# Kernel optimization log

Hardware: AMD Instinct MI355X
Metric: run time of the kernel (lower is better)

## Reference

```python
import jax, jax.numpy as jnp
import numpy as np

HEADS = 16

def setup_inputs() -> dict:
    key = jax.random.key(0)
    k1, k2, k3 = jax.random.split(key, 3)
    B, S, D = 4, 2048, 1024
    x = jax.random.normal(k1, (B, S, D), dtype=jnp.float32)
    w_qkv = jax.random.normal(k2, (D, 3 * D), dtype=jnp.float32) * (D ** -0.5)
    w_out = jax.random.normal(k3, (D, D), dtype=jnp.float32) * (D ** -0.5)
    return {"x": x, "w_qkv": w_qkv, "w_out": w_out}

def reference(x, w_qkv, w_out):
    B, S, D = x.shape
    H = HEADS
    hd = D // H
    qkv = jnp.einsum("bsd,de->bse", x, w_qkv)  # [B,S,3D]
    q, k, v = jnp.split(qkv, 3, axis=-1)
    # [B,S,D] -> [B,H,S,hd]
    q = q.reshape(B, S, H, hd).transpose(0, 2, 1, 3)
    k = k.reshape(B, S, H, hd).transpose(0, 2, 1, 3)
    v = v.reshape(B, S, H, hd).transpose(0, 2, 1, 3)
    scores = jnp.einsum("bhqd,bhkd->bhqk", q, k) / jnp.sqrt(jnp.float32(hd))
    attn = jax.nn.softmax(scores, axis=-1)
    out = jnp.einsum("bhqk,bhkd->bhqd", attn, v)  # [B,H,S,hd]
    out = out.transpose(0, 2, 1, 3).reshape(B, S, D)
    return jnp.einsum("bsd,de->bse", out, w_out)
```

## Files before the change

kernel.cpp:

```cpp
#include <hip/hip_runtime.h>

typedef __bf16 bf16;
typedef __bf16 bfx8 __attribute__((ext_vector_type(8)));
typedef __bf16 bfx4 __attribute__((ext_vector_type(4)));
typedef float f32x4 __attribute__((ext_vector_type(4)));

#define MFMA_BF16 __builtin_amdgcn_mfma_f32_16x16x32_bf16

static constexpr int Bq = 4, Sq = 2048, Dq = 1024, Hq = 16, HDq = 64;
static constexpr int Mq = Bq * Sq;
static constexpr int D3 = 3 * Dq;
static constexpr float L2E = 1.4426950408889634f;
static constexpr float QSC = 0.125f * L2E;

typedef const __attribute__((address_space(1))) void* gas1;
typedef __attribute__((address_space(3))) void* las3;

__device__ __forceinline__ void gload_lds16(const bf16* g, bf16* l) {
    __builtin_amdgcn_global_load_lds((gas1)g, (las3)l, 16, 0, 0);
}

__device__ __forceinline__ float fast_exp2(float x) {
    return __builtin_amdgcn_exp2f(x);
}

__global__ __launch_bounds__(256) void cast_f32_bf16(const float* __restrict__ in,
                                                     bf16* __restrict__ out, int n) {
    int i = (blockIdx.x * 256 + threadIdx.x) * 4;
    if (i + 3 < n) {
        float4 v = *(const float4*)(in + i);
        bfx4 r;
        r[0] = (bf16)v.x; r[1] = (bf16)v.y; r[2] = (bf16)v.z; r[3] = (bf16)v.w;
        *(bfx4*)(out + i) = r;
    }
}

__global__ __launch_bounds__(256) void transpose_cast(const float* __restrict__ in,
                                                      bf16* __restrict__ out, int R, int C) {
    __shared__ float tile[32][33];
    int tx = threadIdx.x, ty = threadIdx.y;
    int c0 = blockIdx.x * 32, r0 = blockIdx.y * 32;
    for (int j = 0; j < 32; j += 8)
        tile[ty + j][tx] = in[(size_t)(r0 + ty + j) * C + c0 + tx];
    __syncthreads();
    for (int j = 0; j < 32; j += 8)
        out[(size_t)(c0 + ty + j) * R + r0 + tx] = (bf16)tile[tx][ty + j];
}

__global__ __launch_bounds__(256) void vtrans(const bf16* __restrict__ qkv,
                                              bf16* __restrict__ Vt) {
    __shared__ bf16 tile[32][33];
    int tx = threadIdx.x, ty = threadIdx.y;
    int c0 = blockIdx.x * 32;
    int s0 = blockIdx.y * 32;
    int b = blockIdx.z;
    for (int j = 0; j < 32; j += 8)
        tile[ty + j][tx] = qkv[(size_t)(b * Sq + s0 + ty + j) * D3 + 2 * Dq + c0 + tx];
    __syncthreads();
    for (int j = 0; j < 32; j += 8)
        Vt[((size_t)b * Dq + c0 + ty + j) * Sq + s0 + tx] = tile[tx][ty + j];
}

template <bool OUT_F32, bool QSCALE>
__global__ __launch_bounds__(256) void gemm_bt(const bf16* __restrict__ A,
                                               const bf16* __restrict__ Bt,
                                               void* __restrict__ Cout,
                                               int M, int N, int K) {
    __shared__ bf16 As[128 * 64];
    __shared__ bf16 Bs[128 * 64];
    int m0 = blockIdx.y * 128;
    int n0 = blockIdx.x * 128;
    int tid = threadIdx.x;
    int lane = tid & 63, wave = tid >> 6;
    int quad = lane >> 4, l16 = lane & 15;
    int wr = wave >> 1, wc = wave & 1;
    int sw = l16 & 7;

    f32x4 acc[4][4] = {};

    for (int k0 = 0; k0 < K; k0 += 64) {
        __syncthreads();
        #pragma unroll
        for (int i = 0; i < 4; i++) {
            int c = i * 256 + tid;
            int row = c >> 3;
            int ch = (c & 7) ^ (row & 7);
            gload_lds16(A + (size_t)(m0 + row) * K + k0 + ch * 8, As + c * 8);
            gload_lds16(Bt + (size_t)(n0 + row) * K + k0 + ch * 8, Bs + c * 8);
        }
        __syncthreads();
        #pragma unroll
        for (int s = 0; s < 2; s++) {
            bfx8 af[4], bfr[4];
            #pragma unroll
            for (int i = 0; i < 4; i++)
                af[i] = *(const bfx8*)(As + (wr * 64 + i * 16 + l16) * 64 +
                                       ((s * 4 + quad) ^ sw) * 8);
            #pragma unroll
            for (int j = 0; j < 4; j++)
                bfr[j] = *(const bfx8*)(Bs + (wc * 64 + j * 16 + l16) * 64 +
                                        ((s * 4 + quad) ^ sw) * 8);
            #pragma unroll
            for (int i = 0; i < 4; i++)
                #pragma unroll
                for (int j = 0; j < 4; j++)
                    acc[i][j] = MFMA_BF16(af[i], bfr[j], acc[i][j], 0, 0, 0);
        }
    }

    #pragma unroll
    for (int i = 0; i < 4; i++)
        #pragma unroll
        for (int j = 0; j < 4; j++) {
            int col = n0 + wc * 64 + j * 16 + l16;
            float scale = (QSCALE && col < Dq) ? QSC : 1.0f;
            #pragma unroll
            for (int r = 0; r < 4; r++) {
                int row = m0 + wr * 64 + i * 16 + quad * 4 + r;
                if (OUT_F32)
                    ((float*)Cout)[(size_t)row * N + col] = acc[i][j][r];
                else
                    ((bf16*)Cout)[(size_t)row * N + col] = (bf16)(acc[i][j][r] * scale);
            }
        }
}

__global__ __launch_bounds__(256, 2) void attn_kernel(const bf16* __restrict__ qkv,
                                                      const bf16* __restrict__ Vt,
                                                      bf16* __restrict__ out) {
    __shared__ bf16 Ks[2][64 * 64];
    __shared__ bf16 Vs[2][64 * 64];
    __shared__ bf16 Ps[4][64 * 64];

    int bid = blockIdx.x;
    int qc = (bid >> 3) & 7;
    int head = (bid & 7) + ((bid >> 6) << 3);
    int h = head & 15, b = head >> 4;
    int tid = threadIdx.x;
    int lane = tid & 63, wave = tid >> 6;
    int quad = lane >> 4, l16 = lane & 15;
    int sw = l16 & 7;

    size_t base = (size_t)b * Sq * D3;
    const bf16* Kbase = qkv + base + Dq + h * HDq;
    const bf16* Vbase = Vt + ((size_t)b * Dq + h * HDq) * Sq;
    int q0 = qc * 256 + wave * 64;

    bfx8 qf[4][2];
    #pragma unroll
    for (int qt = 0; qt < 4; qt++)
        #pragma unroll
        for (int s = 0; s < 2; s++)
            qf[qt][s] = *(const bfx8*)(qkv + base + (size_t)(q0 + qt * 16 + l16) * D3 +
                                       h * HDq + s * 32 + quad * 8);

    bfx8 ones;
    #pragma unroll
    for (int j = 0; j < 8; j++) ones[j] = (bf16)1.0f;

    f32x4 oacc[4][4] = {};
    f32x4 lacc[4] = {};

    int c0 = tid, c1 = tid + 256;
    int r0 = c0 >> 3, ch0 = (c0 & 7) ^ (r0 & 7);
    int r1 = c1 >> 3, ch1 = (c1 & 7) ^ (r1 & 7);

    gload_lds16(Kbase + (size_t)r0 * D3 + ch0 * 8, Ks[0] + c0 * 8);
    gload_lds16(Vbase + (size_t)r0 * Sq + ch0 * 8, Vs[0] + c0 * 8);
    gload_lds16(Kbase + (size_t)r1 * D3 + ch1 * 8, Ks[0] + c1 * 8);
    gload_lds16(Vbase + (size_t)r1 * Sq + ch1 * 8, Vs[0] + c1 * 8);

    for (int i = 0; i < 32; i++) {
        int cur = i & 1;
        __syncthreads();
        if (i + 1 < 32) {
            int k0 = (i + 1) * 64;
            bf16* kd = Ks[cur ^ 1];
            bf16* vd = Vs[cur ^ 1];
            gload_lds16(Kbase + (size_t)(k0 + r0) * D3 + ch0 * 8, kd + c0 * 8);
            gload_lds16(Vbase + (size_t)r0 * Sq + k0 + ch0 * 8, vd + c0 * 8);
            gload_lds16(Kbase + (size_t)(k0 + r1) * D3 + ch1 * 8, kd + c1 * 8);
            gload_lds16(Vbase + (size_t)r1 * Sq + k0 + ch1 * 8, vd + c1 * 8);
        }
        const bf16* K_ = Ks[cur];
        const bf16* V_ = Vs[cur];

        bfx8 kf[4][2];
        #pragma unroll
        for (int t = 0; t < 4; t++) {
            kf[t][0] = *(const bfx8*)(K_ + (t * 16 + l16) * 64 + (quad ^ sw) * 8);
            kf[t][1] = *(const bfx8*)(K_ + (t * 16 + l16) * 64 + ((4 + quad) ^ sw) * 8);
        }

        #pragma unroll
        for (int qt = 0; qt < 4; qt++) {
            f32x4 s[4] = {};
            #pragma unroll
            for (int t = 0; t < 4; t++) {
                s[t] = MFMA_BF16(kf[t][0], qf[qt][0], s[t], 0, 0, 0);
                s[t] = MFMA_BF16(kf[t][1], qf[qt][1], s[t], 0, 0, 0);
            }
            #pragma unroll
            for (int t = 0; t < 4; t++) {
                bfx4 pk;
                #pragma unroll
                for (int r = 0; r < 4; r++)
                    pk[r] = (bf16)fast_exp2(s[t][r]);
                int slot = (2 * t + (quad >> 1)) ^ sw;
                *(bfx4*)(&Ps[wave][(qt * 16 + l16) * 64 + slot * 8 + (quad & 1) * 4]) = pk;
            }
        }

        bfx8 pf[4][2];
        #pragma unroll
        for (int qt = 0; qt < 4; qt++) {
            pf[qt][0] = *(const bfx8*)(&Ps[wave][(qt * 16 + l16) * 64 + (quad ^ sw) * 8]);
            pf[qt][1] = *(const bfx8*)(&Ps[wave][(qt * 16 + l16) * 64 + ((4 + quad) ^ sw) * 8]);
            lacc[qt] = MFMA_BF16(pf[qt][0], ones, lacc[qt], 0, 0, 0);
            lacc[qt] = MFMA_BF16(pf[qt][1], ones, lacc[qt], 0, 0, 0);
        }

        #pragma unroll
        for (int nt = 0; nt < 4; nt++) {
            bfx8 vf0 = *(const bfx8*)(V_ + (nt * 16 + l16) * 64 + (quad ^ sw) * 8);
            bfx8 vf1 = *(const bfx8*)(V_ + (nt * 16 + l16) * 64 + ((4 + quad) ^ sw) * 8);
            #pragma unroll
            for (int qt = 0; qt < 4; qt++) {
                oacc[qt][nt] = MFMA_BF16(pf[qt][0], vf0, oacc[qt][nt], 0, 0, 0);
                oacc[qt][nt] = MFMA_BF16(pf[qt][1], vf1, oacc[qt][nt], 0, 0, 0);
            }
        }
    }

    #pragma unroll
    for (int qt = 0; qt < 4; qt++)
        #pragma unroll
        for (int r = 0; r < 4; r++) {
            int row = q0 + qt * 16 + quad * 4 + r;
            float inv = 1.0f / lacc[qt][r];
            #pragma unroll
            for (int nt = 0; nt < 4; nt++)
                out[((size_t)b * Sq + row) * Dq + h * HDq + nt * 16 + l16] =
                    (bf16)(oacc[qt][nt][r] * inv);
        }
}

extern "C" void kernel_launch(void* const* d_in, const int* in_sizes, int n_in,
                              void* d_out, int out_size, void* d_ws, size_t ws_size,
                              hipStream_t stream) {
    const float* x     = (const float*)d_in[0];
    const float* w_qkv = (const float*)d_in[1];
    const float* w_out = (const float*)d_in[2];
    float* out = (float*)d_out;

    char* ws = (char*)d_ws;
    bf16* x_bf   = (bf16*)ws;
    bf16* wqkvT  = (bf16*)(ws + 16777216);
    bf16* woutT  = (bf16*)(ws + 16777216 + 6291456);
    bf16* qkv    = (bf16*)(ws + 16777216 + 6291456 + 2097152);
    bf16* attn   = (bf16*)(ws + 16777216 + 6291456 + 2097152 + 50331648);
    bf16* Vt     = x_bf;

    cast_f32_bf16<<<(Mq * Dq) / 4 / 256, 256, 0, stream>>>(x, x_bf, Mq * Dq);
    dim3 tb(32, 8);
    transpose_cast<<<dim3(D3 / 32, Dq / 32), tb, 0, stream>>>(w_qkv, wqkvT, Dq, D3);
    transpose_cast<<<dim3(Dq / 32, Dq / 32), tb, 0, stream>>>(w_out, woutT, Dq, Dq);

    gemm_bt<false, true><<<dim3(D3 / 128, Mq / 128), 256, 0, stream>>>(x_bf, wqkvT, qkv, Mq, D3, Dq);

    vtrans<<<dim3(Dq / 32, Sq / 32, Bq), tb, 0, stream>>>(qkv, Vt);

    attn_kernel<<<512, 256, 0, stream>>>(qkv, Vt, attn);

    gemm_bt<true, false><<<dim3(Dq / 128, Mq / 128), 256, 0, stream>>>(attn, woutT, out, Mq, Dq, Dq);
}
```

Baseline: 269.9 us.

## Halve attention query tile per wave and split key block into halves for occupancy

Each wave now handles 32 query rows instead of 64, so the grid doubles to 1024 blocks and launch bounds allow 4 blocks per CU. The 64-key inner step is processed in two 32-key halves, which shrinks the P staging buffer to 32x32 per wave and reduces register pressure. The intent is better latency hiding and fuller use of the CUs. In exchange, each K/V tile loaded into LDS is reused by fewer queries, so global and LDS traffic per FLOP doubles.

New measurement: 266.8 us. Within noise of the previous version (-1.1%).

```diff
diff --git a/kernel.cpp b/kernel.cpp
--- a/kernel.cpp
+++ b/kernel.cpp
@@ -125,30 +125,31 @@
         }
 }
 
-__global__ __launch_bounds__(256, 2) void attn_kernel(const bf16* __restrict__ qkv,
+__global__ __launch_bounds__(256, 4) void attn_kernel(const bf16* __restrict__ qkv,
                                                       const bf16* __restrict__ Vt,
                                                       bf16* __restrict__ out) {
     __shared__ bf16 Ks[2][64 * 64];
     __shared__ bf16 Vs[2][64 * 64];
-    __shared__ bf16 Ps[4][64 * 64];
+    __shared__ bf16 Ps[4][32 * 32];
 
     int bid = blockIdx.x;
-    int qc = (bid >> 3) & 7;
-    int head = (bid & 7) + ((bid >> 6) << 3);
+    int qc = (bid >> 3) & 15;
+    int head = ((bid >> 7) << 3) | (bid & 7);
     int h = head & 15, b = head >> 4;
     int tid = threadIdx.x;
     int lane = tid & 63, wave = tid >> 6;
     int quad = lane >> 4, l16 = lane & 15;
     int sw = l16 & 7;
+    int sw4 = l16 & 3;
 
     size_t base = (size_t)b * Sq * D3;
     const bf16* Kbase = qkv + base + Dq + h * HDq;
     const bf16* Vbase = Vt + ((size_t)b * Dq + h * HDq) * Sq;
-    int q0 = qc * 256 + wave * 64;
-
-    bfx8 qf[4][2];
-    #pragma unroll
-    for (int qt = 0; qt < 4; qt++)
+    int q0 = qc * 128 + wave * 32;
+
+    bfx8 qf[2][2];
+    #pragma unroll
+    for (int qt = 0; qt < 2; qt++)
         #pragma unroll
         for (int s = 0; s < 2; s++)
             qf[qt][s] = *(const bfx8*)(qkv + base + (size_t)(q0 + qt * 16 + l16) * D3 +
@@ -158,8 +159,8 @@
     #pragma unroll
     for (int j = 0; j < 8; j++) ones[j] = (bf16)1.0f;
 
-    f32x4 oacc[4][4] = {};
-    f32x4 lacc[4] = {};
+    f32x4 oacc[2][4] = {};
+    f32x4 lacc[2] = {};
 
     int c0 = tid, c1 = tid + 256;
     int r0 = c0 >> 3, ch0 = (c0 & 7) ^ (r0 & 7);
@@ -185,55 +186,55 @@
         const bf16* K_ = Ks[cur];
         const bf16* V_ = Vs[cur];
 
-        bfx8 kf[4][2];
-        #pragma unroll
-        for (int t = 0; t < 4; t++) {
-            kf[t][0] = *(const bfx8*)(K_ + (t * 16 + l16) * 64 + (quad ^ sw) * 8);
-            kf[t][1] = *(const bfx8*)(K_ + (t * 16 + l16) * 64 + ((4 + quad) ^ sw) * 8);
-        }
-
-        #pragma unroll
-        for (int qt = 0; qt < 4; qt++) {
-            f32x4 s[4] = {};
-            #pragma unroll
-            for (int t = 0; t < 4; t++) {
-                s[t] = MFMA_BF16(kf[t][0], qf[qt][0], s[t], 0, 0, 0);
-                s[t] = MFMA_BF16(kf[t][1], qf[qt][1], s[t], 0, 0, 0);
-            }
-            #pragma unroll
-            for (int t = 0; t < 4; t++) {
-                bfx4 pk;
-                #pragma unroll
-                for (int r = 0; r < 4; r++)
-                    pk[r] = (bf16)fast_exp2(s[t][r]);
-                int slot = (2 * t + (quad >> 1)) ^ sw;
-                *(bfx4*)(&Ps[wave][(qt * 16 + l16) * 64 + slot * 8 + (quad & 1) * 4]) = pk;
-            }
-        }
-
-        bfx8 pf[4][2];
-        #pragma unroll
-        for (int qt = 0; qt < 4; qt++) {
-            pf[qt][0] = *(const bfx8*)(&Ps[wave][(qt * 16 + l16) * 64 + (quad ^ sw) * 8]);
-            pf[qt][1] = *(const bfx8*)(&Ps[wave][(qt * 16 + l16) * 64 + ((4 + quad) ^ sw) * 8]);
-            lacc[qt] = MFMA_BF16(pf[qt][0], ones, lacc[qt], 0, 0, 0);
-            lacc[qt] = MFMA_BF16(pf[qt][1], ones, lacc[qt], 0, 0, 0);
-        }
-
-        #pragma unroll
-        for (int nt = 0; nt < 4; nt++) {
-            bfx8 vf0 = *(const bfx8*)(V_ + (nt * 16 + l16) * 64 + (quad ^ sw) * 8);
-            bfx8 vf1 = *(const bfx8*)(V_ + (nt * 16 + l16) * 64 + ((4 + quad) ^ sw) * 8);
-            #pragma unroll
-            for (int qt = 0; qt < 4; qt++) {
-                oacc[qt][nt] = MFMA_BF16(pf[qt][0], vf0, oacc[qt][nt], 0, 0, 0);
-                oacc[qt][nt] = MFMA_BF16(pf[qt][1], vf1, oacc[qt][nt], 0, 0, 0);
+        #pragma unroll
+        for (int hf = 0; hf < 2; hf++) {
+            bfx8 kf[2][2];
+            #pragma unroll
+            for (int tp = 0; tp < 2; tp++) {
+                int krow = ((2 * hf + tp) * 16 + l16) * 64;
+                kf[tp][0] = *(const bfx8*)(K_ + krow + (quad ^ sw) * 8);
+                kf[tp][1] = *(const bfx8*)(K_ + krow + ((4 + quad) ^ sw) * 8);
+            }
+
+            #pragma unroll
+            for (int qt = 0; qt < 2; qt++) {
+                f32x4 s[2] = {};
+                #pragma unroll
+                for (int tp = 0; tp < 2; tp++) {
+                    s[tp] = MFMA_BF16(kf[tp][0], qf[qt][0], s[tp], 0, 0, 0);
+                    s[tp] = MFMA_BF16(kf[tp][1], qf[qt][1], s[tp], 0, 0, 0);
+                }
+                #pragma unroll
+                for (int tp = 0; tp < 2; tp++) {
+                    bfx4 pk;
+                    #pragma unroll
+                    for (int r = 0; r < 4; r++)
+                        pk[r] = (bf16)fast_exp2(s[tp][r]);
+                    int slot = (2 * tp + (quad >> 1)) ^ sw4;
+                    *(bfx4*)(&Ps[wave][(qt * 16 + l16) * 32 + slot * 8 + (quad & 1) * 4]) = pk;
+                }
+            }
+
+            bfx8 pf[2];
+            #pragma unroll
+            for (int qt = 0; qt < 2; qt++) {
+                pf[qt] = *(const bfx8*)(&Ps[wave][(qt * 16 + l16) * 32 + (quad ^ sw4) * 8]);
+                lacc[qt] = MFMA_BF16(pf[qt], ones, lacc[qt], 0, 0, 0);
+            }
+
+            #pragma unroll
+            for (int nt = 0; nt < 4; nt++) {
+                bfx8 vf = *(const bfx8*)(V_ + (nt * 16 + l16) * 64 +
+                                         ((hf * 4 + quad) ^ sw) * 8);
+                #pragma unroll
+                for (int qt = 0; qt < 2; qt++)
+                    oacc[qt][nt] = MFMA_BF16(pf[qt], vf, oacc[qt][nt], 0, 0, 0);
             }
         }
     }
 
     #pragma unroll
-    for (int qt = 0; qt < 4; qt++)
+    for (int qt = 0; qt < 2; qt++)
         #pragma unroll
         for (int r = 0; r < 4; r++) {
             int row = q0 + qt * 16 + quad * 4 + r;
@@ -270,7 +271,7 @@
 
     vtrans<<<dim3(Dq / 32, Sq / 32, Bq), tb, 0, stream>>>(qkv, Vt);
 
-    attn_kernel<<<512, 256, 0, stream>>>(qkv, Vt, attn);
+    attn_kernel<<<1024, 256, 0, stream>>>(qkv, Vt, attn);
 
     gemm_bt<true, false><<<dim3(Dq / 128, Mq / 128), 256, 0, stream>>>(attn, woutT, out, Mq, Dq, Dq);
 }
```

## Keep softmax probabilities in registers and shrink attention and output GEMM tiles

Applied to the files above, without the earlier changes.

The attention kernel permutes K rows at load time so that the score MFMA output layout directly matches the P operand layout for the PV MFMA. This removes the per-wave LDS round trip for P and the ones-MFMA row sum, which is replaced by register accumulation plus cross-lane shuffles. Blocks shrink to 128 threads with 1024 blocks for more occupancy. The output projection switches to a new 128x64-tile GEMM to get more blocks, at the cost of dropping the double-buffered or larger-tile path and re-reading A more often.

Result: slower. 303.5 us (+12.4%).

```diff
diff --git a/kernel.cpp b/kernel.cpp
--- a/kernel.cpp
+++ b/kernel.cpp
@@ -125,16 +125,80 @@
         }
 }
 
-__global__ __launch_bounds__(256, 2) void attn_kernel(const bf16* __restrict__ qkv,
+__global__ __launch_bounds__(256) void gemm_bt_n64(const bf16* __restrict__ A,
+                                                   const bf16* __restrict__ Bt,
+                                                   float* __restrict__ Cout,
+                                                   int M, int N, int K) {
+    __shared__ bf16 As[128 * 64];
+    __shared__ bf16 Bs[64 * 64];
+    int m0 = blockIdx.y * 128;
+    int n0 = blockIdx.x * 64;
+    int tid = threadIdx.x;
+    int lane = tid & 63, wave = tid >> 6;
+    int quad = lane >> 4, l16 = lane & 15;
+    int wr = wave >> 1, wc = wave & 1;
+    int sw = l16 & 7;
+
+    f32x4 acc[4][2] = {};
+
+    for (int k0 = 0; k0 < K; k0 += 64) {
+        __syncthreads();
+        #pragma unroll
+        for (int i = 0; i < 4; i++) {
+            int c = i * 256 + tid;
+            int row = c >> 3;
+            int ch = (c & 7) ^ (row & 7);
+            gload_lds16(A + (size_t)(m0 + row) * K + k0 + ch * 8, As + c * 8);
+        }
+        #pragma unroll
+        for (int i = 0; i < 2; i++) {
+            int c = i * 256 + tid;
+            int row = c >> 3;
+            int ch = (c & 7) ^ (row & 7);
+            gload_lds16(Bt + (size_t)(n0 + row) * K + k0 + ch * 8, Bs + c * 8);
+        }
+        __syncthreads();
+        #pragma unroll
+        for (int s = 0; s < 2; s++) {
+            bfx8 af[4], bfr[2];
+            #pragma unroll
+            for (int i = 0; i < 4; i++)
+                af[i] = *(const bfx8*)(As + (wr * 64 + i * 16 + l16) * 64 +
+                                       ((s * 4 + quad) ^ sw) * 8);
+            #pragma unroll
+            for (int j = 0; j < 2; j++)
+                bfr[j] = *(const bfx8*)(Bs + (wc * 32 + j * 16 + l16) * 64 +
+                                        ((s * 4 + quad) ^ sw) * 8);
+            #pragma unroll
+            for (int i = 0; i < 4; i++)
+                #pragma unroll
+                for (int j = 0; j < 2; j++)
+                    acc[i][j] = MFMA_BF16(af[i], bfr[j], acc[i][j], 0, 0, 0);
+        }
+    }
+
+    #pragma unroll
+    for (int i = 0; i < 4; i++)
+        #pragma unroll
+        for (int j = 0; j < 2; j++) {
+            int col = n0 + wc * 32 + j * 16 + l16;
+            #pragma unroll
+            for (int r = 0; r < 4; r++) {
+                int row = m0 + wr * 64 + i * 16 + quad * 4 + r;
+                Cout[(size_t)row * N + col] = acc[i][j][r];
+            }
+        }
+}
+
+__global__ __launch_bounds__(128, 3) void attn_kernel(const bf16* __restrict__ qkv,
                                                       const bf16* __restrict__ Vt,
                                                       bf16* __restrict__ out) {
     __shared__ bf16 Ks[2][64 * 64];
     __shared__ bf16 Vs[2][64 * 64];
-    __shared__ bf16 Ps[4][64 * 64];
 
     int bid = blockIdx.x;
-    int qc = (bid >> 3) & 7;
-    int head = (bid & 7) + ((bid >> 6) << 3);
+    int head = bid & 63;
+    int qc = bid >> 6;
     int h = head & 15, b = head >> 4;
     int tid = threadIdx.x;
     int lane = tid & 63, wave = tid >> 6;
@@ -144,7 +208,7 @@
     size_t base = (size_t)b * Sq * D3;
     const bf16* Kbase = qkv + base + Dq + h * HDq;
     const bf16* Vbase = Vt + ((size_t)b * Dq + h * HDq) * Sq;
-    int q0 = qc * 256 + wave * 64;
+    int q0 = qc * 128 + wave * 64;
 
     bfx8 qf[4][2];
     #pragma unroll
@@ -154,21 +218,25 @@
             qf[qt][s] = *(const bfx8*)(qkv + base + (size_t)(q0 + qt * 16 + l16) * D3 +
                                        h * HDq + s * 32 + quad * 8);
 
-    bfx8 ones;
-    #pragma unroll
-    for (int j = 0; j < 8; j++) ones[j] = (bf16)1.0f;
-
     f32x4 oacc[4][4] = {};
-    f32x4 lacc[4] = {};
-
-    int c0 = tid, c1 = tid + 256;
-    int r0 = c0 >> 3, ch0 = (c0 & 7) ^ (r0 & 7);
-    int r1 = c1 >> 3, ch1 = (c1 & 7) ^ (r1 & 7);
-
-    gload_lds16(Kbase + (size_t)r0 * D3 + ch0 * 8, Ks[0] + c0 * 8);
-    gload_lds16(Vbase + (size_t)r0 * Sq + ch0 * 8, Vs[0] + c0 * 8);
-    gload_lds16(Kbase + (size_t)r1 * D3 + ch1 * 8, Ks[0] + c1 * 8);
-    gload_lds16(Vbase + (size_t)r1 * Sq + ch1 * 8, Vs[0] + c1 * 8);
+    float lsum[4] = {0.f, 0.f, 0.f, 0.f};
+
+    int src_r[4], src_ch[4], kperm[4];
+    #pragma unroll
+    for (int j = 0; j < 4; j++) {
+        int c = tid + j * 128;
+        int r = c >> 3;
+        src_r[j] = r;
+        src_ch[j] = (c & 7) ^ (r & 7);
+        kperm[j] = 32 * (r >> 5) + 4 * ((r >> 4) & 1) + 8 * ((r & 15) >> 2) + (r & 3);
+    }
+
+    #pragma unroll
+    for (int j = 0; j < 4; j++) {
+        int c = tid + j * 128;
+        gload_lds16(Kbase + (size_t)kperm[j] * D3 + src_ch[j] * 8, Ks[0] + c * 8);
+        gload_lds16(Vbase + (size_t)src_r[j] * Sq + src_ch[j] * 8, Vs[0] + c * 8);
+    }
 
     for (int i = 0; i < 32; i++) {
         int cur = i & 1;
@@ -177,59 +245,76 @@
             int k0 = (i + 1) * 64;
             bf16* kd = Ks[cur ^ 1];
             bf16* vd = Vs[cur ^ 1];
-            gload_lds16(Kbase + (size_t)(k0 + r0) * D3 + ch0 * 8, kd + c0 * 8);
-            gload_lds16(Vbase + (size_t)r0 * Sq + k0 + ch0 * 8, vd + c0 * 8);
-            gload_lds16(Kbase + (size_t)(k0 + r1) * D3 + ch1 * 8, kd + c1 * 8);
-            gload_lds16(Vbase + (size_t)r1 * Sq + k0 + ch1 * 8, vd + c1 * 8);
+            #pragma unroll
+            for (int j = 0; j < 4; j++) {
+                int c = tid + j * 128;
+                gload_lds16(Kbase + (size_t)(k0 + kperm[j]) * D3 + src_ch[j] * 8, kd + c * 8);
+                gload_lds16(Vbase + (size_t)src_r[j] * Sq + k0 + src_ch[j] * 8, vd + c * 8);
+            }
         }
         const bf16* K_ = Ks[cur];
         const bf16* V_ = Vs[cur];
 
-        bfx8 kf[4][2];
-        #pragma unroll
-        for (int t = 0; t < 4; t++) {
-            kf[t][0] = *(const bfx8*)(K_ + (t * 16 + l16) * 64 + (quad ^ sw) * 8);
-            kf[t][1] = *(const bfx8*)(K_ + (t * 16 + l16) * 64 + ((4 + quad) ^ sw) * 8);
-        }
-
-        #pragma unroll
-        for (int qt = 0; qt < 4; qt++) {
-            f32x4 s[4] = {};
-            #pragma unroll
-            for (int t = 0; t < 4; t++) {
-                s[t] = MFMA_BF16(kf[t][0], qf[qt][0], s[t], 0, 0, 0);
-                s[t] = MFMA_BF16(kf[t][1], qf[qt][1], s[t], 0, 0, 0);
-            }
-            #pragma unroll
-            for (int t = 0; t < 4; t++) {
-                bfx4 pk;
-                #pragma unroll
-                for (int r = 0; r < 4; r++)
-                    pk[r] = (bf16)fast_exp2(s[t][r]);
-                int slot = (2 * t + (quad >> 1)) ^ sw;
-                *(bfx4*)(&Ps[wave][(qt * 16 + l16) * 64 + slot * 8 + (quad & 1) * 4]) = pk;
-            }
-        }
-
-        bfx8 pf[4][2];
-        #pragma unroll
-        for (int qt = 0; qt < 4; qt++) {
-            pf[qt][0] = *(const bfx8*)(&Ps[wave][(qt * 16 + l16) * 64 + (quad ^ sw) * 8]);
-            pf[qt][1] = *(const bfx8*)(&Ps[wave][(qt * 16 + l16) * 64 + ((4 + quad) ^ sw) * 8]);
-            lacc[qt] = MFMA_BF16(pf[qt][0], ones, lacc[qt], 0, 0, 0);
-            lacc[qt] = MFMA_BF16(pf[qt][1], ones, lacc[qt], 0, 0, 0);
-        }
-
-        #pragma unroll
-        for (int nt = 0; nt < 4; nt++) {
-            bfx8 vf0 = *(const bfx8*)(V_ + (nt * 16 + l16) * 64 + (quad ^ sw) * 8);
-            bfx8 vf1 = *(const bfx8*)(V_ + (nt * 16 + l16) * 64 + ((4 + quad) ^ sw) * 8);
-            #pragma unroll
-            for (int qt = 0; qt < 4; qt++) {
-                oacc[qt][nt] = MFMA_BF16(pf[qt][0], vf0, oacc[qt][nt], 0, 0, 0);
-                oacc[qt][nt] = MFMA_BF16(pf[qt][1], vf1, oacc[qt][nt], 0, 0, 0);
-            }
-        }
+        #pragma unroll
+        for (int kt = 0; kt < 2; kt++) {
+            bfx4 plo[4], phi[4];
+            {
+                const bf16* Kh = K_ + (2 * kt) * 16 * 64;
+                bfx8 k0f = *(const bfx8*)(Kh + l16 * 64 + (quad ^ sw) * 8);
+                bfx8 k1f = *(const bfx8*)(Kh + l16 * 64 + ((4 + quad) ^ sw) * 8);
+                #pragma unroll
+                for (int qt = 0; qt < 4; qt++) {
+                    f32x4 s = {};
+                    s = MFMA_BF16(k0f, qf[qt][0], s, 0, 0, 0);
+                    s = MFMA_BF16(k1f, qf[qt][1], s, 0, 0, 0);
+                    #pragma unroll
+                    for (int r = 0; r < 4; r++) {
+                        float e = fast_exp2(s[r]);
+                        plo[qt][r] = (bf16)e;
+                        lsum[qt] += e;
+                    }
+                }
+            }
+            {
+                const bf16* Kh = K_ + (2 * kt + 1) * 16 * 64;
+                bfx8 k0f = *(const bfx8*)(Kh + l16 * 64 + (quad ^ sw) * 8);
+                bfx8 k1f = *(const bfx8*)(Kh + l16 * 64 + ((4 + quad) ^ sw) * 8);
+                #pragma unroll
+                for (int qt = 0; qt < 4; qt++) {
+                    f32x4 s = {};
+                    s = MFMA_BF16(k0f, qf[qt][0], s, 0, 0, 0);
+                    s = MFMA_BF16(k1f, qf[qt][1], s, 0, 0, 0);
+                    #pragma unroll
+                    for (int r = 0; r < 4; r++) {
+                        float e = fast_exp2(s[r]);
+                        phi[qt][r] = (bf16)e;
+                        lsum[qt] += e;
+                    }
+                }
+            }
+            bfx8 p8[4];
+            #pragma unroll
+            for (int qt = 0; qt < 4; qt++)
+                p8[qt] = __builtin_shufflevector(plo[qt], phi[qt], 0, 1, 2, 3, 4, 5, 6, 7);
+
+            #pragma unroll
+            for (int nt = 0; nt < 4; nt++) {
+                bfx8 vf = *(const bfx8*)(V_ + (nt * 16 + l16) * 64 +
+                                         ((4 * kt + quad) ^ sw) * 8);
+                #pragma unroll
+                for (int qt = 0; qt < 4; qt++)
+                    oacc[qt][nt] = MFMA_BF16(p8[qt], vf, oacc[qt][nt], 0, 0, 0);
+            }
+        }
+    }
+
+    float lfull[4];
+    #pragma unroll
+    for (int qt = 0; qt < 4; qt++) {
+        float v = lsum[qt];
+        v += __shfl_xor(v, 16);
+        v += __shfl_xor(v, 32);
+        lfull[qt] = v;
     }
 
     #pragma unroll
@@ -237,7 +322,7 @@
         #pragma unroll
         for (int r = 0; r < 4; r++) {
             int row = q0 + qt * 16 + quad * 4 + r;
-            float inv = 1.0f / lacc[qt][r];
+            float inv = 1.0f / __shfl(lfull[qt], quad * 4 + r);
             #pragma unroll
             for (int nt = 0; nt < 4; nt++)
                 out[((size_t)b * Sq + row) * Dq + h * HDq + nt * 16 + l16] =
@@ -270,7 +355,7 @@
 
     vtrans<<<dim3(Dq / 32, Sq / 32, Bq), tb, 0, stream>>>(qkv, Vt);
 
-    attn_kernel<<<512, 256, 0, stream>>>(qkv, Vt, attn);
-
-    gemm_bt<true, false><<<dim3(Dq / 128, Mq / 128), 256, 0, stream>>>(attn, woutT, out, Mq, Dq, Dq);
-}
+    attn_kernel<<<1024, 128, 0, stream>>>(qkv, Vt, attn);
+
+    gemm_bt_n64<<<dim3(Dq / 64, Mq / 128), 256, 0, stream>>>(attn, woutT, out, Mq, Dq, Dq);
+}
```
